# Optimization experiments

Hardware: AMD Instinct MI355X
Metric: run time of the kernel (lower is better)

## Reference

```python
import jax, jax.numpy as jnp
import numpy as np

N, E, IN, OUT = 50000, 1600000, 64, 64
DIM, K = 2, 5          # pseudo-coordinate dim, kernel size per dim
KP = K ** DIM          # 25 kernel weight matrices
S = 2 ** DIM           # 4 non-zero linear B-spline basis products per edge
# bit pattern per basis product: bits[s, d] in {0,1}
_BITS = np.array([[(s >> d) & 1 for d in range(DIM)] for s in range(S)], dtype=np.int32)
_OFFS = np.array([K ** (DIM - 1 - d) for d in range(DIM)], dtype=np.int32)  # row-major flatten


def setup_inputs() -> dict:
    key = jax.random.key(0)
    ks = jax.random.split(key, 6)
    x = jax.random.normal(ks[0], (N, IN), dtype=jnp.float32)
    edge_index = jax.random.randint(ks[1], (2, E), 0, N)
    pseudo = jax.random.uniform(ks[2], (E, DIM), dtype=jnp.float32)
    bnd = 1.0 / np.sqrt(KP * IN)  # matches uniform(size) init in reset_parameters
    weight = jax.random.uniform(ks[3], (KP, IN, OUT), dtype=jnp.float32, minval=-bnd, maxval=bnd)
    root_weight = jax.random.uniform(ks[4], (IN, OUT), dtype=jnp.float32, minval=-bnd, maxval=bnd)
    bias = jax.random.uniform(ks[5], (OUT,), dtype=jnp.float32, minval=-bnd, maxval=bnd)
    return {"x": x, "edge_index": edge_index, "pseudo": pseudo,
            "weight": weight, "root_weight": root_weight, "bias": bias}


def _basis_and_index(pseudo):
    # open B-spline, degree 1: scale by (K - 1)
    v = pseudo * jnp.asarray(K - 1, pseudo.dtype)          # [E, DIM]
    lo = jnp.floor(v)
    frac = v - lo                                          # [E, DIM]
    lo = lo.astype(jnp.int32)
    bits = jnp.asarray(_BITS)                              # [S, DIM]
    # basis[e, s] = prod_d (frac if bit else 1-frac)
    terms = jnp.where(bits[None].astype(bool), frac[:, None, :], 1.0 - frac[:, None, :])
    basis = jnp.prod(terms, axis=-1)                       # [E, S]
    idx_d = (lo[:, None, :] + bits[None]) % K              # [E, S, DIM]; wrap is harmless (basis=0 there)
    idx = jnp.sum(idx_d * jnp.asarray(_OFFS), axis=-1)     # [E, S] flat weight index in [0, KP)
    return basis, idx


def reference(x, edge_index, pseudo, weight, root_weight, bias):
    row, col = edge_index[0], edge_index[1]                # row = target, col = source
    basis, idx = _basis_and_index(pseudo)                  # [E,S], [E,S]
    x_src = x[col]                                         # [E, IN] gather
    # Accumulate basis-weighted source features per (target node, kernel index),
    # then apply the dense [KP, IN, OUT] weights once (same math, no [E,IN,OUT] blowup).
    acc = jnp.zeros((N * KP, IN), x.dtype)
    for s in range(S):  # S=4, fixed structural loop
        acc = acc + jax.ops.segment_sum(basis[:, s:s + 1] * x_src,
                                        row * KP + idx[:, s], num_segments=N * KP)
    out = jnp.einsum('nki,kio->no', acc.reshape(N, KP, IN), weight)  # [N, OUT]
    deg = jax.ops.segment_sum(jnp.ones((E,), x.dtype), row, num_segments=N)
    out = out / jnp.clip(deg, 1.0)[:, None]                # mean over neighbors (1/N(i))
    return out + x @ root_weight + bias
```

## Files before the change

kernel.cpp:

```cpp
#include <hip/hip_runtime.h>
#include <hip/hip_fp16.h>
#include <hip/hip_bf16.h>


#define NN    50000
#define EE    1600000
#define NPB   16
#define KD    1664
#define ASTB  1672
#define CAP   56
#define OFCAP 16384

typedef unsigned short ushort_t;
typedef __attribute__((ext_vector_type(8))) short short8;
typedef __attribute__((ext_vector_type(4))) float f32x4;

static __device__ __forceinline__ ushort_t f2bf(float f) {
  union { float f; unsigned u; } v; v.f = f;
  return (ushort_t)((v.u + 0x7fffu + ((v.u >> 16) & 1u)) >> 16);
}
static __device__ __forceinline__ unsigned pk2bf(float a, float b) {
  __hip_bfloat162 h = __float22bfloat162_rn(make_float2(a, b));
  union { __hip_bfloat162 h; unsigned u; } cv; cv.h = h; return cv.u;
}
union S8 { short8 s; unsigned u[4]; };

__global__ void k_wt(const float* __restrict__ w, const float* __restrict__ root,
                     ushort_t* __restrict__ wt) {
  int idx = blockIdx.x * 256 + threadIdx.x;
  if (idx >= 64 * KD) return;
  int o = idx / KD, k = idx - o * KD;
  wt[idx] = (k < 1600) ? f2bf(w[k * 64 + o]) : f2bf(root[(k - 1600) * 64 + o]);
}

__global__ void k_xb(const float* __restrict__ x, ushort_t* __restrict__ xb) {
  int i = blockIdx.x * 256 + threadIdx.x;
  if (i < NN * 64) xb[i] = f2bf(x[i]);
}

__global__ void k_rec(const int* __restrict__ ei, const float* __restrict__ pseudo,
                      int* __restrict__ cursor, uint2* __restrict__ recs,
                      uint4* __restrict__ ofl) {
  int e = blockIdx.x * 256 + threadIdx.x;
  if (e >= EE) return;
  int row = ei[e], col = ei[EE + e];
  float2 pv = ((const float2*)pseudo)[e];
  float v0 = pv.x * 4.0f, v1 = pv.y * 4.0f;
  int slot = atomicAdd(&cursor[row], 1);
  if (slot < CAP) {
    unsigned h0 = __half_as_ushort(__float2half(v0));
    unsigned h1 = __half_as_ushort(__float2half(v1));
    recs[row * CAP + slot] = make_uint2((unsigned)col, h0 | (h1 << 16));
  } else {
    int o = atomicAdd(&cursor[NN], 1);
    if (o < OFCAP)
      ofl[o] = make_uint4((unsigned)row, (unsigned)col,
                          __float_as_uint(v0), __float_as_uint(v1));
  }
}

template <bool XBF>
__global__ __launch_bounds__(1024) void k_main(
    const uint2* __restrict__ recs, const int* __restrict__ cursor,
    const uint4* __restrict__ ofl,
    const float* __restrict__ x, const ushort_t* __restrict__ xb,
    const ushort_t* __restrict__ wt, const float* __restrict__ bias,
    float* __restrict__ out) {
  __shared__ ushort_t accS[NPB * ASTB];
  __shared__ float    outp[4 * NPB * 64];
  __shared__ float    sinv[NPB];
  const int tid = threadIdx.x;
  const int lane = tid & 63;
  const int w = tid >> 6;
  const int nb = blockIdx.x * NPB;
  const int node = nb + w;

  const int dg = cursor[node];
  const int m = min(dg, CAP);
  const float dcf = (float)max(dg, 1);
  if (lane == 0) sinv[w] = 1.0f / dcf;
  accS[w * ASTB + 1600 + lane] = f2bf(x[(size_t)node * 64 + lane] * dcf);

  const int m15 = lane & 15, quad = lane >> 4;
  const float r0f = (float)(m15 / 5),        c0f = (float)(m15 % 5);
  const float r1f = (float)((16 + m15) / 5), c1f = (float)((16 + m15) % 5);

  f32x4 acc[2][4];
#pragma unroll
  for (int a = 0; a < 2; ++a)
#pragma unroll
    for (int b = 0; b < 4; ++b) acc[a][b] = (f32x4){0.f, 0.f, 0.f, 0.f};

  const uint2* bket = recs + (size_t)node * CAP;
  for (int e0 = 0; e0 < m; e0 += 32) {
    float a0f[8], a1f[8];
    float bfv[4][8];
    unsigned bu[4][8];
#pragma unroll
    for (int j = 0; j < 8; ++j) {
      int e = e0 + quad * 8 + j;
      int ec = min(e, m - 1);
      uint2 rc = bket[ec];
      float msk = (e < m) ? 1.0f : 0.0f;
      float v0 = __half2float(__ushort_as_half((ushort_t)(rc.y & 0xFFFFu)));
      float v1 = __half2float(__ushort_as_half((ushort_t)(rc.y >> 16)));
      float h00 = fmaxf(0.f, 1.f - fabsf(v0 - r0f));
      float h01 = fmaxf(0.f, 1.f - fabsf(v1 - c0f));
      float h10 = fmaxf(0.f, 1.f - fabsf(v0 - r1f));
      float h11 = fmaxf(0.f, 1.f - fabsf(v1 - c1f));
      a0f[j] = h00 * h01 * msk;
      a1f[j] = h10 * h11 * msk;
      if (XBF) {
        const ushort_t* xr = xb + (size_t)rc.x * 64 + m15;
        bu[0][j] = xr[0];
        bu[1][j] = xr[16];
        bu[2][j] = xr[32];
        bu[3][j] = xr[48];
      } else {
        const float* xr = x + (size_t)rc.x * 64 + m15;
        bfv[0][j] = xr[0];
        bfv[1][j] = xr[16];
        bfv[2][j] = xr[32];
        bfv[3][j] = xr[48];
      }
    }
    S8 aT0, aT1, bT[4];
#pragma unroll
    for (int p = 0; p < 4; ++p) {
      aT0.u[p] = pk2bf(a0f[2 * p], a0f[2 * p + 1]);
      aT1.u[p] = pk2bf(a1f[2 * p], a1f[2 * p + 1]);
#pragma unroll
      for (int t = 0; t < 4; ++t)
        bT[t].u[p] = XBF ? (bu[t][2 * p] | (bu[t][2 * p + 1] << 16))
                         : pk2bf(bfv[t][2 * p], bfv[t][2 * p + 1]);
    }
#pragma unroll
    for (int t = 0; t < 4; ++t) {
      acc[0][t] = __builtin_amdgcn_mfma_f32_16x16x32_bf16(aT0.s, bT[t].s, acc[0][t], 0, 0, 0);
      acc[1][t] = __builtin_amdgcn_mfma_f32_16x16x32_bf16(aT1.s, bT[t].s, acc[1][t], 0, 0, 0);
    }
  }

  {
    int ofc = min(cursor[NN], OFCAP);
    for (int i = 0; i < ofc; ++i) {
      uint4 r = ofl[i];
      if ((int)r.x != node) continue;
      float v0 = __uint_as_float(r.z), v1 = __uint_as_float(r.w);
      float h00 = fmaxf(0.f, 1.f - fabsf(v0 - r0f));
      float h01 = fmaxf(0.f, 1.f - fabsf(v1 - c0f));
      float h10 = fmaxf(0.f, 1.f - fabsf(v0 - r1f));
      float h11 = fmaxf(0.f, 1.f - fabsf(v1 - c1f));
      float mk = (quad == 0) ? 1.0f : 0.0f;
      S8 aT0, aT1, bT[4];
#pragma unroll
      for (int p = 0; p < 4; ++p) { aT0.u[p] = 0; aT1.u[p] = 0; }
      aT0.u[0] = pk2bf(h00 * h01 * mk, 0.0f);
      aT1.u[0] = pk2bf(h10 * h11 * mk, 0.0f);
      const float* xr = x + (size_t)r.y * 64 + m15;
#pragma unroll
      for (int t = 0; t < 4; ++t) {
        float xv = xr[16 * t];
#pragma unroll
        for (int p = 0; p < 4; ++p) bT[t].u[p] = pk2bf(xv, xv);
      }
#pragma unroll
      for (int t = 0; t < 4; ++t) {
        acc[0][t] = __builtin_amdgcn_mfma_f32_16x16x32_bf16(aT0.s, bT[t].s, acc[0][t], 0, 0, 0);
        acc[1][t] = __builtin_amdgcn_mfma_f32_16x16x32_bf16(aT1.s, bT[t].s, acc[1][t], 0, 0, 0);
      }
    }
  }

#pragma unroll
  for (int mt = 0; mt < 2; ++mt)
#pragma unroll
    for (int r = 0; r < 4; ++r) {
      int kp = mt * 16 + quad * 4 + r;
      if (kp < 25) {
#pragma unroll
        for (int nt = 0; nt < 4; ++nt)
          accS[w * ASTB + kp * 64 + nt * 16 + m15] = f2bf(acc[mt][nt][r]);
      }
    }
  __syncthreads();

  {
    const int ntile = w & 3, kh = w >> 2;
    const int m2 = lane & 15, quad2 = lane >> 4;
    const int nn2 = ntile * 16 + m2;
    f32x4 d = {0.0f, 0.0f, 0.0f, 0.0f};
    const ushort_t* ab = &accS[m2 * ASTB + kh * 416 + quad2 * 8];
    const ushort_t* wb = &wt[(size_t)nn2 * KD + kh * 416 + quad2 * 8];
    for (int kk = 0; kk < 13; ++kk) {
      short8 af = *(const short8*)(ab + kk * 32);
      short8 bf = *(const short8*)(wb + kk * 32);
      d = __builtin_amdgcn_mfma_f32_16x16x32_bf16(af, bf, d, 0, 0, 0);
    }
#pragma unroll
    for (int r = 0; r < 4; ++r)
      outp[kh * (NPB * 64) + (quad2 * 4 + r) * 64 + ntile * 16 + m2] = d[r];
  }
  __syncthreads();

  {
    float conv = outp[0 * (NPB * 64) + w * 64 + lane]
               + outp[1 * (NPB * 64) + w * 64 + lane]
               + outp[2 * (NPB * 64) + w * 64 + lane]
               + outp[3 * (NPB * 64) + w * 64 + lane];
    out[(size_t)node * 64 + lane] = conv * sinv[w] + bias[lane];
  }
}

__global__ void k_sentinel(float* __restrict__ out) {
  int i = blockIdx.x * 256 + threadIdx.x;
  if (i < NN * 64) out[i] = 1000.0f;
}

extern "C" void kernel_launch(void* const* d_in, const int* in_sizes, int n_in,
                              void* d_out, int out_size, void* d_ws, size_t ws_size,
                              hipStream_t stream) {
  const float* x      = (const float*)d_in[0];
  const int*   ei     = (const int*)d_in[1];
  const float* pseudo = (const float*)d_in[2];
  const float* w      = (const float*)d_in[3];
  const float* root   = (const float*)d_in[4];
  const float* bias   = (const float*)d_in[5];
  float* out = (float*)d_out;
  (void)in_sizes; (void)n_in; (void)out_size;

  char* ws = (char*)d_ws;
  size_t off = 0;
  auto alloc = [&](size_t bytes) { size_t r = off; off += (bytes + 511) & ~(size_t)511; return r; };
  ushort_t* wt     = (ushort_t*)(ws + alloc((size_t)64 * KD * 2));
  int*      cursor = (int*)(ws + alloc((size_t)(NN + 1) * 4));
  uint4*    ofl    = (uint4*)(ws + alloc((size_t)OFCAP * 16));
  uint2*    recs   = (uint2*)(ws + alloc((size_t)NN * CAP * 8));
  size_t baseNeed  = off;
  ushort_t* xb     = (ushort_t*)(ws + alloc((size_t)NN * 64 * 2));
  size_t fullNeed  = off;

  if (ws_size < baseNeed) {
    k_sentinel<<<(NN * 64 + 255) / 256, 256, 0, stream>>>(out);
    return;
  }
  const bool useXB = (ws_size >= fullNeed);

  k_wt<<<(64 * KD + 255) / 256, 256, 0, stream>>>(w, root, wt);
  hipMemsetAsync(cursor, 0, (size_t)(NN + 1) * 4, stream);
  if (useXB) k_xb<<<(NN * 64 + 255) / 256, 256, 0, stream>>>(x, xb);
  k_rec<<<(EE + 255) / 256, 256, 0, stream>>>(ei, pseudo, cursor, recs, ofl);
  if (useXB)
    k_main<true><<<NN / NPB, 1024, 0, stream>>>(recs, cursor, ofl, x, xb, wt, bias, out);
  else
    k_main<false><<<NN / NPB, 1024, 0, stream>>>(recs, cursor, ofl, x, xb, wt, bias, out);
}
```

Measured before the change: 352.8 us.

## Fuse prep kernels into one launch and shuffle-broadcast edge records in main loop

Merges the weight-transpose, x-to-bf16 and edge-bucketing kernels into a single launch that dispatches on block index, and vectorises the x conversion to 8 elements per thread. In the main kernel, each lane loads one edge record once, and the records are broadcast with wave shuffles, replacing eight redundant per-lane record loads per 32-edge chunk. The MFMA block is also wrapped in raised wave priority. This cuts launch overhead and record-load traffic, at the cost of extra shuffle instructions and a larger combined prep kernel.

After: 352.8 us. About the same (-0.0%).

```diff
diff --git a/kernel.cpp b/kernel.cpp
--- a/kernel.cpp
+++ b/kernel.cpp
@@ -11,6 +11,10 @@
 #define CAP   56
 #define OFCAP 16384
 
+#define REC_B 6250
+#define XB_B  1563
+#define WT_B  104
+
 typedef unsigned short ushort_t;
 typedef __attribute__((ext_vector_type(8))) short short8;
 typedef __attribute__((ext_vector_type(4))) float f32x4;
@@ -25,37 +29,51 @@
 }
 union S8 { short8 s; unsigned u[4]; };
 
-__global__ void k_wt(const float* __restrict__ w, const float* __restrict__ root,
-                     ushort_t* __restrict__ wt) {
-  int idx = blockIdx.x * 256 + threadIdx.x;
-  if (idx >= 64 * KD) return;
-  int o = idx / KD, k = idx - o * KD;
-  wt[idx] = (k < 1600) ? f2bf(w[k * 64 + o]) : f2bf(root[(k - 1600) * 64 + o]);
-}
-
-__global__ void k_xb(const float* __restrict__ x, ushort_t* __restrict__ xb) {
-  int i = blockIdx.x * 256 + threadIdx.x;
-  if (i < NN * 64) xb[i] = f2bf(x[i]);
-}
-
-__global__ void k_rec(const int* __restrict__ ei, const float* __restrict__ pseudo,
-                      int* __restrict__ cursor, uint2* __restrict__ recs,
-                      uint4* __restrict__ ofl) {
-  int e = blockIdx.x * 256 + threadIdx.x;
-  if (e >= EE) return;
-  int row = ei[e], col = ei[EE + e];
-  float2 pv = ((const float2*)pseudo)[e];
-  float v0 = pv.x * 4.0f, v1 = pv.y * 4.0f;
-  int slot = atomicAdd(&cursor[row], 1);
-  if (slot < CAP) {
-    unsigned h0 = __half_as_ushort(__float2half(v0));
-    unsigned h1 = __half_as_ushort(__float2half(v1));
-    recs[row * CAP + slot] = make_uint2((unsigned)col, h0 | (h1 << 16));
+__global__ __launch_bounds__(256) void k_prep(
+    const int* __restrict__ ei, const float* __restrict__ pseudo,
+    int* __restrict__ cursor, uint2* __restrict__ recs, uint4* __restrict__ ofl,
+    const float* __restrict__ x, ushort_t* __restrict__ xb,
+    const float* __restrict__ w, const float* __restrict__ root,
+    ushort_t* __restrict__ wt, int useXB) {
+  const int b = blockIdx.x;
+  if (b < REC_B) {
+    int e = b * 256 + threadIdx.x;
+    int row = ei[e], col = ei[EE + e];
+    float2 pv = ((const float2*)pseudo)[e];
+    float v0 = pv.x * 4.0f, v1 = pv.y * 4.0f;
+    int slot = atomicAdd(&cursor[row], 1);
+    if (slot < CAP) {
+      unsigned h0 = __half_as_ushort(__float2half(v0));
+      unsigned h1 = __half_as_ushort(__float2half(v1));
+      recs[row * CAP + slot] = make_uint2((unsigned)col, h0 | (h1 << 16));
+    } else {
+      int o = atomicAdd(&cursor[NN], 1);
+      if (o < OFCAP)
+        ofl[o] = make_uint4((unsigned)row, (unsigned)col,
+                            __float_as_uint(v0), __float_as_uint(v1));
+    }
+  } else if (b < REC_B + XB_B) {
+    if (!useXB) return;
+    int t = (b - REC_B) * 256 + threadIdx.x;
+    if (t < NN * 8) {
+      const float4* xp = (const float4*)x + (size_t)t * 2;
+      float4 aa = xp[0], bb = xp[1];
+      S8 o;
+      o.u[0] = pk2bf(aa.x, aa.y); o.u[1] = pk2bf(aa.z, aa.w);
+      o.u[2] = pk2bf(bb.x, bb.y); o.u[3] = pk2bf(bb.z, bb.w);
+      ((short8*)xb)[t] = o.s;
+    }
   } else {
-    int o = atomicAdd(&cursor[NN], 1);
-    if (o < OFCAP)
-      ofl[o] = make_uint4((unsigned)row, (unsigned)col,
-                          __float_as_uint(v0), __float_as_uint(v1));
+    int t = (b - REC_B - XB_B) * 256 + threadIdx.x;
+    int idx = t * 4;
+    if (idx < 64 * KD) {
+      int o = idx / KD, k = idx - o * KD;
+#pragma unroll
+      for (int q = 0; q < 4; ++q) {
+        int kk = k + q;
+        wt[idx + q] = (kk < 1600) ? f2bf(w[kk * 64 + o]) : f2bf(root[(kk - 1600) * 64 + o]);
+      }
+    }
   }
 }
 
@@ -92,53 +110,59 @@
     for (int b = 0; b < 4; ++b) acc[a][b] = (f32x4){0.f, 0.f, 0.f, 0.f};
 
   const uint2* bket = recs + (size_t)node * CAP;
+  unsigned rcx = 0u, rcy = 0x7C007C00u;
+  if (lane < m) { uint2 rr = bket[lane]; rcx = rr.x; rcy = rr.y; }
+
   for (int e0 = 0; e0 < m; e0 += 32) {
-    float a0f[8], a1f[8];
-    float bfv[4][8];
-    unsigned bu[4][8];
+    const int eb = e0 + quad * 8;
+    unsigned cj[8], pj[8];
 #pragma unroll
     for (int j = 0; j < 8; ++j) {
-      int e = e0 + quad * 8 + j;
-      int ec = min(e, m - 1);
-      uint2 rc = bket[ec];
-      float msk = (e < m) ? 1.0f : 0.0f;
-      float v0 = __half2float(__ushort_as_half((ushort_t)(rc.y & 0xFFFFu)));
-      float v1 = __half2float(__ushort_as_half((ushort_t)(rc.y >> 16)));
-      float h00 = fmaxf(0.f, 1.f - fabsf(v0 - r0f));
-      float h01 = fmaxf(0.f, 1.f - fabsf(v1 - c0f));
-      float h10 = fmaxf(0.f, 1.f - fabsf(v0 - r1f));
-      float h11 = fmaxf(0.f, 1.f - fabsf(v1 - c1f));
-      a0f[j] = h00 * h01 * msk;
-      a1f[j] = h10 * h11 * msk;
+      cj[j] = (unsigned)__shfl((int)rcx, eb + j);
+      pj[j] = (unsigned)__shfl((int)rcy, eb + j);
+    }
+    S8 aT0, aT1, bT[4];
+#pragma unroll
+    for (int p = 0; p < 4; ++p) {
       if (XBF) {
-        const ushort_t* xr = xb + (size_t)rc.x * 64 + m15;
-        bu[0][j] = xr[0];
-        bu[1][j] = xr[16];
-        bu[2][j] = xr[32];
-        bu[3][j] = xr[48];
+        const ushort_t* xr0 = xb + (size_t)cj[2 * p] * 64 + m15;
+        const ushort_t* xr1 = xb + (size_t)cj[2 * p + 1] * 64 + m15;
+        unsigned l0 = xr0[0], l1 = xr0[16], l2 = xr0[32], l3 = xr0[48];
+        unsigned h0 = xr1[0], h1 = xr1[16], h2 = xr1[32], h3 = xr1[48];
+        bT[0].u[p] = l0 | (h0 << 16);
+        bT[1].u[p] = l1 | (h1 << 16);
+        bT[2].u[p] = l2 | (h2 << 16);
+        bT[3].u[p] = l3 | (h3 << 16);
       } else {
-        const float* xr = x + (size_t)rc.x * 64 + m15;
-        bfv[0][j] = xr[0];
-        bfv[1][j] = xr[16];
-        bfv[2][j] = xr[32];
-        bfv[3][j] = xr[48];
-      }
-    }
-    S8 aT0, aT1, bT[4];
+        const float* xr0 = x + (size_t)cj[2 * p] * 64 + m15;
+        const float* xr1 = x + (size_t)cj[2 * p + 1] * 64 + m15;
+        bT[0].u[p] = pk2bf(xr0[0],  xr1[0]);
+        bT[1].u[p] = pk2bf(xr0[16], xr1[16]);
+        bT[2].u[p] = pk2bf(xr0[32], xr1[32]);
+        bT[3].u[p] = pk2bf(xr0[48], xr1[48]);
+      }
+    }
 #pragma unroll
     for (int p = 0; p < 4; ++p) {
-      aT0.u[p] = pk2bf(a0f[2 * p], a0f[2 * p + 1]);
-      aT1.u[p] = pk2bf(a1f[2 * p], a1f[2 * p + 1]);
-#pragma unroll
-      for (int t = 0; t < 4; ++t)
-        bT[t].u[p] = XBF ? (bu[t][2 * p] | (bu[t][2 * p + 1] << 16))
-                         : pk2bf(bfv[t][2 * p], bfv[t][2 * p + 1]);
-    }
+      float a0[2], a1[2];
+#pragma unroll
+      for (int q = 0; q < 2; ++q) {
+        unsigned pv = pj[2 * p + q];
+        float v0 = __half2float(__ushort_as_half((ushort_t)(pv & 0xFFFFu)));
+        float v1 = __half2float(__ushort_as_half((ushort_t)(pv >> 16)));
+        a0[q] = fmaxf(0.f, 1.f - fabsf(v0 - r0f)) * fmaxf(0.f, 1.f - fabsf(v1 - c0f));
+        a1[q] = fmaxf(0.f, 1.f - fabsf(v0 - r1f)) * fmaxf(0.f, 1.f - fabsf(v1 - c1f));
+      }
+      aT0.u[p] = pk2bf(a0[0], a0[1]);
+      aT1.u[p] = pk2bf(a1[0], a1[1]);
+    }
+    __builtin_amdgcn_s_setprio(1);
 #pragma unroll
     for (int t = 0; t < 4; ++t) {
       acc[0][t] = __builtin_amdgcn_mfma_f32_16x16x32_bf16(aT0.s, bT[t].s, acc[0][t], 0, 0, 0);
       acc[1][t] = __builtin_amdgcn_mfma_f32_16x16x32_bf16(aT1.s, bT[t].s, acc[1][t], 0, 0, 0);
     }
+    __builtin_amdgcn_s_setprio(0);
   }
 
   {
@@ -244,12 +268,11 @@
     k_sentinel<<<(NN * 64 + 255) / 256, 256, 0, stream>>>(out);
     return;
   }
-  const bool useXB = (ws_size >= fullNeed);
-
-  k_wt<<<(64 * KD + 255) / 256, 256, 0, stream>>>(w, root, wt);
+  const int useXB = (ws_size >= fullNeed) ? 1 : 0;
+
   hipMemsetAsync(cursor, 0, (size_t)(NN + 1) * 4, stream);
-  if (useXB) k_xb<<<(NN * 64 + 255) / 256, 256, 0, stream>>>(x, xb);
-  k_rec<<<(EE + 255) / 256, 256, 0, stream>>>(ei, pseudo, cursor, recs, ofl);
+  k_prep<<<REC_B + XB_B + WT_B, 256, 0, stream>>>(ei, pseudo, cursor, recs, ofl,
+                                                  x, xb, w, root, wt, useXB);
   if (useXB)
     k_main<true><<<NN / NPB, 1024, 0, stream>>>(recs, cursor, ofl, x, xb, wt, bias, out);
   else
```
